# Kernel tuning notes

Measured on AMD Instinct MI355X. Metric: run time of the kernel, lower is better.

The kernel has to match this reference:

```python
import jax, jax.numpy as jnp
import numpy as np

B = 65536
CEP_ORDER = 99          # M
IR_LENGTH = 512         # N


def setup_inputs() -> dict:
    key = jax.random.key(0)
    # scale cepstral coeffs like real cepstra (decaying with quefrency) for stability
    scale = 0.5 / (1.0 + jnp.arange(CEP_ORDER + 1, dtype=jnp.float32))
    c = jax.random.normal(key, (B, CEP_ORDER + 1), dtype=jnp.float32) * scale
    return {"c": c}


def reference(c):
    # Oppenheim recursion: h[0] = exp(c[0]); h[n] = (1/n) sum_{m=1}^{min(n,M)} m*c[m]*h[n-m]
    Bc, M1 = c.shape
    M = M1 - 1
    N = IR_LENGTH
    arange = jnp.arange(1, M + 1, dtype=c.dtype)
    c1f = (c[:, 1:] * arange)[:, ::-1]        # flipped weighted cepstrum, [B, M]
    h0 = jnp.exp(c[:, 0])                      # [B]
    # buffer holds h[n-M : n]; zeros for negative indices
    buf0 = jnp.concatenate([jnp.zeros((Bc, M - 1), c.dtype), h0[:, None]], axis=1)

    def step(buf, n):
        hn = jnp.einsum('bm,bm->b', buf, c1f) / n      # [B]
        buf = jnp.concatenate([buf[:, 1:], hn[:, None]], axis=1)
        return buf, hn

    ns = jnp.arange(1, N, dtype=c.dtype)
    _, hs = jax.lax.scan(step, buf0, ns)               # hs: [N-1, B]
    h = jnp.concatenate([h0[:, None], hs.T], axis=1)   # [B, N]
    return h
```

## Files before the change

### kernel.cpp

```cpp
#include <hip/hip_runtime.h>
#include <math.h>


#define NROWS   64
#define STRIDE  129

__device__ __forceinline__ float dpp_xor1(float x) {
    return __int_as_float(__builtin_amdgcn_mov_dpp(__float_as_int(x), 0xB1, 0xF, 0xF, false));
}
__device__ __forceinline__ float dpp_xor2(float x) {
    return __int_as_float(__builtin_amdgcn_mov_dpp(__float_as_int(x), 0x4E, 0xF, 0xF, false));
}
__device__ __forceinline__ float dpp_shr1(float x) {
    return __int_as_float(__builtin_amdgcn_mov_dpp(__float_as_int(x), 0x111, 0xF, 0xF, false));
}

__global__ __launch_bounds__(256, 4)
void cep2ir_kernel(const float* __restrict__ c, float* __restrict__ out) {
    __shared__ float stage[NROWS * STRIDE];
    const int t = threadIdx.x;
    const int l = t & 3;
    const int lrow = t >> 2;
    const bool isBase = (l == 0);
    const int rowbase = blockIdx.x * NROWS;
    const float* cb = c + (size_t)(rowbase + lrow) * 100;
    float* outb = out + (size_t)rowbase * 512;

    float e[28];
    {
        const float4* c4 = reinterpret_cast<const float4*>(cb);
        const int b0 = 6 * l + (l == 3 ? 1 : 0);
#pragma unroll
        for (int i = 0; i < 7; ++i) {
            int blk = b0 + i;
            if (l == 3 && i == 6) blk = 24;
            const float4 v = c4[blk];
            e[4 * i + 0] = v.x; e[4 * i + 1] = v.y;
            e[4 * i + 2] = v.z; e[4 * i + 3] = v.w;
        }
    }
    float w[25];
    {
        const float lf = (float)l;
#pragma unroll
        for (int k = 0; k < 25; ++k) {
            const float ce = (l == 0) ? e[k + 1] : (l == 1) ? e[k + 2]
                           : (l == 2) ? e[k + 3] : e[k];
            w[k] = ce * (25.0f * lf + (float)(k + 1));
        }
        if (l == 3) w[24] = 0.0f;
    }

    const float h0 = expf(e[0]);

    float hh[41];
#pragma unroll
    for (int k = 0; k < 41; ++k) hh[k] = 0.0f;
    hh[16] = isBase ? h0 : 0.0f;

    if (isBase) stage[lrow * STRIDE] = h0;

    float fn = 1.0f;
    float carry = 0.0f;

#pragma unroll 1
    for (int p = 0; p < 4; ++p) {
        float* sp = &stage[lrow * STRIDE + 1];
#pragma unroll 1
        for (int gg = 0; gg < 8; ++gg) {
            float rn[16];
#pragma unroll
            for (int j = 0; j < 16; ++j) rn[j] = __builtin_amdgcn_rcpf(fn + (float)j);

#pragma unroll
            for (int j = 0; j < 16; ++j) {
                float a0 = 0.f, a1 = 0.f;
#pragma unroll
                for (int k = 0; k < 25; ++k) {
                    if ((k & 1) == 0) a0 = __builtin_fmaf(w[k], hh[k + 16 - j], a0);
                    else              a1 = __builtin_fmaf(w[k], hh[k + 16 - j], a1);
                }
                float s = a0 + a1;
                s += dpp_xor1(s);
                s += dpp_xor2(s);
                const float hn = s * rn[j];
                hh[15 - j] = isBase ? hn : hh[15 - j];
                if (j == 15) carry = hn;
            }
            if (isBase) {
#pragma unroll
                for (int j = 0; j < 16; ++j) sp[j] = hh[15 - j];
            }
            float bv[16];
#pragma unroll
            for (int jj = 0; jj < 16; ++jj) bv[jj] = dpp_shr1(hh[9 + jj]);
#pragma unroll
            for (int k = 40; k >= 16; --k) hh[k] = hh[k - 16];
#pragma unroll
            for (int jj = 0; jj < 16; ++jj) hh[jj] = bv[jj];
            fn += 16.0f;
            sp += 16;
        }
        __syncthreads();
#pragma unroll 1
        for (int i = 0; i < 32; ++i) {
            const int idx = i * 256 + t;
            const int r = idx >> 7;
            const int cc = idx & 127;
            outb[(size_t)r * 512 + p * 128 + cc] = stage[r * STRIDE + cc];
        }
        __syncthreads();
        if (p < 3 && isBase) stage[lrow * STRIDE] = carry;
    }
}

extern "C" void kernel_launch(void* const* d_in, const int* in_sizes, int n_in,
                              void* d_out, int out_size, void* d_ws, size_t ws_size,
                              hipStream_t stream) {
    const float* c = (const float*)d_in[0];
    float* out = (float*)d_out;
    cep2ir_kernel<<<1024, 256, 0, stream>>>(c, out);
}
```

Before: 123.2 us.

## Process two rows per lane group with packed FP32 FMA

Each 4-lane group now runs the recursion for two batch rows at once, holding weights and history as float2 vectors and using v_pk_fma_f32 so one instruction does two FMAs. Rows per block double to 128 and the grid halves to 512 blocks, with launch bounds lowered to 2. This amortises per-step overhead (reciprocals, DPP reductions, shifts) across two rows and targets higher FMA throughput. In exchange it roughly doubles register use and LDS per block, which lowers occupancy, and it leaves only 512 blocks to spread across the GPU.

```diff
diff --git a/kernel.cpp b/kernel.cpp
--- a/kernel.cpp
+++ b/kernel.cpp
@@ -2,8 +2,10 @@
 #include <math.h>
 
 
-#define NROWS   64
+#define NROWS   128
 #define STRIDE  129
+
+typedef float f2 __attribute__((ext_vector_type(2)));
 
 __device__ __forceinline__ float dpp_xor1(float x) {
     return __int_as_float(__builtin_amdgcn_mov_dpp(__float_as_int(x), 0xB1, 0xF, 0xF, false));
@@ -14,58 +16,67 @@
 __device__ __forceinline__ float dpp_shr1(float x) {
     return __int_as_float(__builtin_amdgcn_mov_dpp(__float_as_int(x), 0x111, 0xF, 0xF, false));
 }
+__device__ __forceinline__ f2 pk_fma(f2 a, f2 b, f2 c) {
+    f2 d;
+    asm("v_pk_fma_f32 %0, %1, %2, %3" : "=v"(d) : "v"(a), "v"(b), "v"(c));
+    return d;
+}
 
-__global__ __launch_bounds__(256, 4)
+__global__ __launch_bounds__(256, 2)
 void cep2ir_kernel(const float* __restrict__ c, float* __restrict__ out) {
     __shared__ float stage[NROWS * STRIDE];
     const int t = threadIdx.x;
     const int l = t & 3;
-    const int lrow = t >> 2;
+    const int q = t >> 2;
     const bool isBase = (l == 0);
+    const int r0 = 2 * q;
     const int rowbase = blockIdx.x * NROWS;
-    const float* cb = c + (size_t)(rowbase + lrow) * 100;
     float* outb = out + (size_t)rowbase * 512;
 
-    float e[28];
+    f2 w2[25];
+    f2 h02;
     {
-        const float4* c4 = reinterpret_cast<const float4*>(cb);
-        const int b0 = 6 * l + (l == 3 ? 1 : 0);
 #pragma unroll
-        for (int i = 0; i < 7; ++i) {
-            int blk = b0 + i;
-            if (l == 3 && i == 6) blk = 24;
-            const float4 v = c4[blk];
-            e[4 * i + 0] = v.x; e[4 * i + 1] = v.y;
-            e[4 * i + 2] = v.z; e[4 * i + 3] = v.w;
+        for (int r = 0; r < 2; ++r) {
+            const float* cb = c + (size_t)(rowbase + r0 + r) * 100;
+            const float4* c4 = reinterpret_cast<const float4*>(cb);
+            float e[28];
+            const int b0 = 6 * l + (l == 3 ? 1 : 0);
+#pragma unroll
+            for (int i = 0; i < 7; ++i) {
+                int blk = b0 + i;
+                if (l == 3 && i == 6) blk = 24;
+                const float4 v = c4[blk];
+                e[4 * i + 0] = v.x; e[4 * i + 1] = v.y;
+                e[4 * i + 2] = v.z; e[4 * i + 3] = v.w;
+            }
+            const float lf = (float)l;
+#pragma unroll
+            for (int k = 0; k < 25; ++k) {
+                const float ce = (l == 0) ? e[k + 1] : (l == 1) ? e[k + 2]
+                               : (l == 2) ? e[k + 3] : e[k];
+                const float wk = ce * (25.0f * lf + (float)(k + 1));
+                if (r == 0) w2[k].x = wk; else w2[k].y = wk;
+            }
+            const float h0 = expf(e[0]);
+            if (r == 0) h02.x = h0; else h02.y = h0;
         }
-    }
-    float w[25];
-    {
-        const float lf = (float)l;
-#pragma unroll
-        for (int k = 0; k < 25; ++k) {
-            const float ce = (l == 0) ? e[k + 1] : (l == 1) ? e[k + 2]
-                           : (l == 2) ? e[k + 3] : e[k];
-            w[k] = ce * (25.0f * lf + (float)(k + 1));
-        }
-        if (l == 3) w[24] = 0.0f;
+        if (l == 3) { w2[24].x = 0.0f; w2[24].y = 0.0f; }
     }
 
-    const float h0 = expf(e[0]);
+    f2 hh2[41];
+#pragma unroll
+    for (int k = 0; k < 41; ++k) { hh2[k].x = 0.0f; hh2[k].y = 0.0f; }
+    if (isBase) hh2[16] = h02;
 
-    float hh[41];
-#pragma unroll
-    for (int k = 0; k < 41; ++k) hh[k] = 0.0f;
-    hh[16] = isBase ? h0 : 0.0f;
-
-    if (isBase) stage[lrow * STRIDE] = h0;
+    float* sp0 = &stage[r0 * STRIDE];
+    if (isBase) { sp0[0] = h02.x; sp0[STRIDE] = h02.y; }
 
     float fn = 1.0f;
-    float carry = 0.0f;
+    f2 carry; carry.x = 0.0f; carry.y = 0.0f;
 
 #pragma unroll 1
     for (int p = 0; p < 4; ++p) {
-        float* sp = &stage[lrow * STRIDE + 1];
 #pragma unroll 1
         for (int gg = 0; gg < 8; ++gg) {
             float rn[16];
@@ -74,43 +85,53 @@
 
 #pragma unroll
             for (int j = 0; j < 16; ++j) {
-                float a0 = 0.f, a1 = 0.f;
+                f2 a0, a1;
+                a0.x = 0.f; a0.y = 0.f; a1.x = 0.f; a1.y = 0.f;
 #pragma unroll
                 for (int k = 0; k < 25; ++k) {
-                    if ((k & 1) == 0) a0 = __builtin_fmaf(w[k], hh[k + 16 - j], a0);
-                    else              a1 = __builtin_fmaf(w[k], hh[k + 16 - j], a1);
+                    if ((k & 1) == 0) a0 = pk_fma(w2[k], hh2[k + 16 - j], a0);
+                    else              a1 = pk_fma(w2[k], hh2[k + 16 - j], a1);
                 }
-                float s = a0 + a1;
-                s += dpp_xor1(s);
-                s += dpp_xor2(s);
-                const float hn = s * rn[j];
-                hh[15 - j] = isBase ? hn : hh[15 - j];
+                f2 s = a0 + a1;
+                f2 tt;
+                tt.x = dpp_xor1(s.x); tt.y = dpp_xor1(s.y); s += tt;
+                tt.x = dpp_xor2(s.x); tt.y = dpp_xor2(s.y); s += tt;
+                f2 hn;
+                hn.x = s.x * rn[j]; hn.y = s.y * rn[j];
+                hh2[15 - j].x = isBase ? hn.x : hh2[15 - j].x;
+                hh2[15 - j].y = isBase ? hn.y : hh2[15 - j].y;
                 if (j == 15) carry = hn;
             }
             if (isBase) {
+                float* sc = sp0 + 1 + 16 * gg;
 #pragma unroll
-                for (int j = 0; j < 16; ++j) sp[j] = hh[15 - j];
+                for (int j = 0; j < 16; ++j) {
+                    sc[j] = hh2[15 - j].x;
+                    sc[STRIDE + j] = hh2[15 - j].y;
+                }
             }
-            float bv[16];
+            f2 bv[16];
 #pragma unroll
-            for (int jj = 0; jj < 16; ++jj) bv[jj] = dpp_shr1(hh[9 + jj]);
+            for (int jj = 0; jj < 16; ++jj) {
+                bv[jj].x = dpp_shr1(hh2[9 + jj].x);
+                bv[jj].y = dpp_shr1(hh2[9 + jj].y);
+            }
 #pragma unroll
-            for (int k = 40; k >= 16; --k) hh[k] = hh[k - 16];
+            for (int k = 40; k >= 16; --k) hh2[k] = hh2[k - 16];
 #pragma unroll
-            for (int jj = 0; jj < 16; ++jj) hh[jj] = bv[jj];
+            for (int jj = 0; jj < 16; ++jj) hh2[jj] = bv[jj];
             fn += 16.0f;
-            sp += 16;
         }
         __syncthreads();
 #pragma unroll 1
-        for (int i = 0; i < 32; ++i) {
+        for (int i = 0; i < 64; ++i) {
             const int idx = i * 256 + t;
             const int r = idx >> 7;
             const int cc = idx & 127;
             outb[(size_t)r * 512 + p * 128 + cc] = stage[r * STRIDE + cc];
         }
         __syncthreads();
-        if (p < 3 && isBase) stage[lrow * STRIDE] = carry;
+        if (p < 3 && isBase) { sp0[0] = carry.x; sp0[STRIDE] = carry.y; }
     }
 }
 
@@ -119,5 +140,5 @@
                               hipStream_t stream) {
     const float* c = (const float*)d_in[0];
     float* out = (float*)d_out;
-    cep2ir_kernel<<<1024, 256, 0, stream>>>(c, out);
+    cep2ir_kernel<<<512, 256, 0, stream>>>(c, out);
 }
```

Result: faster. 118.3 us (-4.0%).

## Double-buffer output staging and overlap global stores with recurrence compute

Applied to the files above, without the earlier changes.

Replaces the single 128-column staging buffer with two 64-column buffers, so the copy of one 64-column chunk to global memory is split across the two 32-step groups of the next chunk. This overlaps the stores with the recurrence instead of stalling on them. Reciprocals 1/n are now precomputed into a shared table and read as float4, and the register window grows to 32 steps per group with lane 1 also holding early values. Stores use float2 and there is one barrier per chunk. This adds register pressure from the larger hh window and extra DPP shifts.

```diff
diff --git a/kernel.cpp b/kernel.cpp
--- a/kernel.cpp
+++ b/kernel.cpp
@@ -3,7 +3,7 @@
 
 
 #define NROWS   64
-#define STRIDE  129
+#define STRIDE  66
 
 __device__ __forceinline__ float dpp_xor1(float x) {
     return __int_as_float(__builtin_amdgcn_mov_dpp(__float_as_int(x), 0xB1, 0xF, 0xF, false));
@@ -14,17 +14,30 @@
 __device__ __forceinline__ float dpp_shr1(float x) {
     return __int_as_float(__builtin_amdgcn_mov_dpp(__float_as_int(x), 0x111, 0xF, 0xF, false));
 }
+__device__ __forceinline__ float dpp_shr2(float x) {
+    return __int_as_float(__builtin_amdgcn_mov_dpp(__float_as_int(x), 0x112, 0xF, 0xF, false));
+}
+__device__ __forceinline__ float dpp_bcast0(float x) {
+    return __int_as_float(__builtin_amdgcn_mov_dpp(__float_as_int(x), 0x00, 0xF, 0xF, false));
+}
 
 __global__ __launch_bounds__(256, 4)
 void cep2ir_kernel(const float* __restrict__ c, float* __restrict__ out) {
-    __shared__ float stage[NROWS * STRIDE];
+    __shared__ float buf[2][NROWS * STRIDE];
+    __shared__ float4 rn4[136];
     const int t = threadIdx.x;
     const int l = t & 3;
     const int lrow = t >> 2;
-    const bool isBase = (l == 0);
     const int rowbase = blockIdx.x * NROWS;
     const float* cb = c + (size_t)(rowbase + lrow) * 100;
     float* outb = out + (size_t)rowbase * 512;
+
+    {
+        float* rt = reinterpret_cast<float*>(rn4);
+        rt[t]       = __builtin_amdgcn_rcpf((float)(t + 1));
+        rt[t + 256] = __builtin_amdgcn_rcpf((float)(t + 257));
+        if (t < 32) rt[t + 512] = 1.0f;
+    }
 
     float e[28];
     {
@@ -51,66 +64,94 @@
         if (l == 3) w[24] = 0.0f;
     }
 
-    const float h0 = expf(e[0]);
+    const float h0 = dpp_bcast0(expf(e[0]));
 
-    float hh[41];
+    float hh[57];
 #pragma unroll
-    for (int k = 0; k < 41; ++k) hh[k] = 0.0f;
-    hh[16] = isBase ? h0 : 0.0f;
+    for (int k = 0; k < 57; ++k) hh[k] = 0.0f;
+    hh[32] = (l == 0) ? h0 : 0.0f;
+    hh[7]  = (l == 1) ? h0 : 0.0f;
 
-    if (isBase) stage[lrow * STRIDE] = h0;
+    float prev = h0;
+    __syncthreads();
 
-    float fn = 1.0f;
-    float carry = 0.0f;
+    float4 r4a = rn4[0];
+    float4 r4b;
 
 #pragma unroll 1
-    for (int p = 0; p < 4; ++p) {
-        float* sp = &stage[lrow * STRIDE + 1];
+    for (int p = 0; p < 8; ++p) {
 #pragma unroll 1
-        for (int gg = 0; gg < 8; ++gg) {
-            float rn[16];
+        for (int g = 0; g < 2; ++g) {
+            const int gidx = 2 * p + g;
+            const float4* rnp = &rn4[8 * gidx];
+            if (p > 0) {
+                const float* fb = buf[(p & 1) ^ 1];
+                const int colbase = 64 * (p - 1);
+                const int fr = t >> 5;
+                const int fc = (t & 31) << 1;
 #pragma unroll
-            for (int j = 0; j < 16; ++j) rn[j] = __builtin_amdgcn_rcpf(fn + (float)j);
-
+                for (int i = 0; i < 4; ++i) {
+                    const int r = 32 * g + 8 * i + fr;
+                    const float2 v = *reinterpret_cast<const float2*>(&fb[r * STRIDE + fc]);
+                    *reinterpret_cast<float2*>(&outb[(size_t)r * 512 + colbase + fc]) = v;
+                }
+            }
 #pragma unroll
-            for (int j = 0; j < 16; ++j) {
+            for (int j = 0; j < 32; ++j) {
+                if ((j & 3) == 0) {
+                    const int q = j >> 2;
+                    if (q & 1) r4a = rnp[q + 1]; else r4b = rnp[q + 1];
+                }
                 float a0 = 0.f, a1 = 0.f;
 #pragma unroll
-                for (int k = 0; k < 25; ++k) {
-                    if ((k & 1) == 0) a0 = __builtin_fmaf(w[k], hh[k + 16 - j], a0);
-                    else              a1 = __builtin_fmaf(w[k], hh[k + 16 - j], a1);
+                for (int k = 24; k >= 0; --k) {
+                    if ((k & 1) == 0) a0 = __builtin_fmaf(w[k], hh[k + 32 - j], a0);
+                    else              a1 = __builtin_fmaf(w[k], hh[k + 32 - j], a1);
                 }
                 float s = a0 + a1;
                 s += dpp_xor1(s);
                 s += dpp_xor2(s);
-                const float hn = s * rn[j];
-                hh[15 - j] = isBase ? hn : hh[15 - j];
-                if (j == 15) carry = hn;
+                const float4& rq = (j & 4) ? r4b : r4a;
+                const float rn = (j & 2) ? ((j & 1) ? rq.w : rq.z)
+                                         : ((j & 1) ? rq.y : rq.x);
+                const float hn = s * rn;
+                hh[31 - j] = (l == 0) ? hn : hh[31 - j];
+                if (j < 6) hh[6 - j] = (l == 1) ? hn : hh[6 - j];
             }
-            if (isBase) {
+            if (l == 0) {
+                float* sc = &buf[p & 1][lrow * STRIDE + 32 * g];
+                float2 v0; v0.x = prev; v0.y = hh[31];
+                *reinterpret_cast<float2*>(&sc[0]) = v0;
 #pragma unroll
-                for (int j = 0; j < 16; ++j) sp[j] = hh[15 - j];
+                for (int i = 1; i < 16; ++i) {
+                    float2 v; v.x = hh[32 - 2 * i]; v.y = hh[31 - 2 * i];
+                    *reinterpret_cast<float2*>(&sc[2 * i]) = v;
+                }
             }
-            float bv[16];
+            prev = hh[0];
+            float bv1[25], bv2[6];
 #pragma unroll
-            for (int jj = 0; jj < 16; ++jj) bv[jj] = dpp_shr1(hh[9 + jj]);
+            for (int d = 0; d < 25; ++d) bv1[d] = dpp_shr1(hh[d]);
 #pragma unroll
-            for (int k = 40; k >= 16; --k) hh[k] = hh[k - 16];
+            for (int d = 0; d < 6; ++d)  bv2[d] = dpp_shr2(hh[19 + d]);
 #pragma unroll
-            for (int jj = 0; jj < 16; ++jj) hh[jj] = bv[jj];
-            fn += 16.0f;
-            sp += 16;
+            for (int k = 56; k >= 32; --k) hh[k] = hh[k - 32];
+#pragma unroll
+            for (int d = 0; d < 25; ++d) hh[7 + d] = bv1[d];
+#pragma unroll
+            for (int d = 0; d < 6; ++d)  hh[1 + d] = bv2[d];
         }
         __syncthreads();
+    }
+    {
+        const int fr = t >> 5;
+        const int fc = (t & 31) << 1;
 #pragma unroll 1
-        for (int i = 0; i < 32; ++i) {
-            const int idx = i * 256 + t;
-            const int r = idx >> 7;
-            const int cc = idx & 127;
-            outb[(size_t)r * 512 + p * 128 + cc] = stage[r * STRIDE + cc];
+        for (int i = 0; i < 8; ++i) {
+            const int r = 8 * i + fr;
+            const float2 v = *reinterpret_cast<const float2*>(&buf[1][r * STRIDE + fc]);
+            *reinterpret_cast<float2*>(&outb[(size_t)r * 512 + 448 + fc]) = v;
         }
-        __syncthreads();
-        if (p < 3 && isBase) stage[lrow * STRIDE] = carry;
     }
 }
 
```

New measurement: 113.5 us. -7.9%, faster.
